# Performance work log

Hardware: AMD Instinct MI355X
Metric: run time of the kernel (lower is better)

The kernel has to match this reference:

```python
import jax, jax.numpy as jnp
import numpy as np

B, C, H, W = 8, 512, 32, 32
N_HEADS, HEAD_CH = 8, 64
INNER = N_HEADS * HEAD_CH  # 512
GROUPS = 32
EPS = 1e-5


def setup_inputs() -> dict:
    key = jax.random.key(0)
    ks = jax.random.split(key, 12)
    s = 0.02
    return {
        "x": jax.random.normal(ks[0], (B, C, H, W), jnp.float32),
        "c": jax.random.normal(ks[1], (B, C, H, W), jnp.float32),  # unused by module
        "gn_gamma": 1.0 + 0.1 * jax.random.normal(ks[2], (C,), jnp.float32),
        "gn_beta": 0.1 * jax.random.normal(ks[3], (C,), jnp.float32),
        "Wq": s * jax.random.normal(ks[4], (INNER, C), jnp.float32),
        "bq": s * jax.random.normal(ks[5], (INNER,), jnp.float32),
        "Wk": s * jax.random.normal(ks[6], (INNER, C), jnp.float32),
        "bk": s * jax.random.normal(ks[7], (INNER,), jnp.float32),
        "Wv": s * jax.random.normal(ks[8], (INNER, C), jnp.float32),
        "bv": s * jax.random.normal(ks[9], (INNER,), jnp.float32),
        "Wo": s * jax.random.normal(ks[10], (C, INNER), jnp.float32),
        "bo": s * jax.random.normal(ks[11], (C,), jnp.float32),
    }


def group_norm(x, gamma, beta):
    b, c, h, w = x.shape
    xg = x.reshape(b, GROUPS, c // GROUPS, h, w)
    mean = xg.mean(axis=(2, 3, 4), keepdims=True)
    var = xg.var(axis=(2, 3, 4), keepdims=True)
    xn = ((xg - mean) * jax.lax.rsqrt(var + EPS)).reshape(b, c, h, w)
    return xn * gamma[None, :, None, None] + beta[None, :, None, None]


def reference(x, c, gn_gamma, gn_beta, Wq, bq, Wk, bk, Wv, bv, Wo, bo):
    b, ch, h, w = x.shape
    L = h * w
    x_in = x
    xn = group_norm(x, gn_gamma, gn_beta).reshape(b, ch, L)  # b c l
    # 1x1 Conv1d == channel-wise linear
    q = jnp.einsum('oc,bcl->bol', Wq, xn) + bq[None, :, None]
    k = jnp.einsum('oc,bcl->bol', Wk, xn) + bk[None, :, None]
    v = jnp.einsum('oc,bcl->bol', Wv, xn) + bv[None, :, None]
    d = INNER // N_HEADS
    q = q.reshape(b * N_HEADS, d, L)
    k = k.reshape(b * N_HEADS, d, L)
    v = v.reshape(b * N_HEADS, d, L)
    scale = 1.0 / np.sqrt(np.sqrt(d))
    attn_map = jnp.einsum('bct,bcs->bts', q * scale, k * scale)  # (b*n) t s
    weight = jax.nn.softmax(attn_map.astype(jnp.float32), axis=-1).astype(attn_map.dtype)
    a = jnp.einsum('bts,bcs->bct', weight, v)  # (b*n) d t
    a = a.reshape(b, INNER, L)
    out = jnp.einsum('oc,bcl->bol', Wo, a) + bo[None, :, None]
    out = out.reshape(b, ch, h, w) + x_in
    return out, attn_map
```

## Files before the change

kernel.cpp:

```cpp
#include <hip/hip_runtime.h>
#include <math.h>

#define B_      8
#define C_      512
#define L_      1024
#define NH_     8
#define D_      64
#define BH_     64
#define GROUPS_ 32
#define CPG_    16
#define EPS_    1e-5f

typedef __attribute__((ext_vector_type(8))) short bf16x8;
typedef __attribute__((ext_vector_type(4))) float f32x4;

__device__ __forceinline__ unsigned short f2bf(float f) {
  union { float f; unsigned u; } v; v.f = f;
  unsigned r = v.u + 0x7FFFu + ((v.u >> 16) & 1u);
  return (unsigned short)(r >> 16);
}

__device__ __forceinline__ void gload_lds16(const unsigned short* g,
                                            unsigned short* l) {
  __builtin_amdgcn_global_load_lds(
      (const __attribute__((address_space(1))) void*)g,
      (__attribute__((address_space(3))) void*)l, 16, 0, 0);
}

__global__ void __launch_bounds__(256) gn_kernel(
    const float* __restrict__ x, const float* __restrict__ gamma,
    const float* __restrict__ beta, unsigned short* __restrict__ xn_t) {
  int b = blockIdx.x >> 5, g = blockIdx.x & 31;
  int tid = threadIdx.x;
  const float* xp = x + ((size_t)b * C_ + g * CPG_) * L_;
  f32x4 vals[CPG_];
  float s = 0.f, ss = 0.f;
#pragma unroll
  for (int c = 0; c < CPG_; ++c) {
    f32x4 v = *(const f32x4*)&xp[(size_t)c * L_ + tid * 4];
    vals[c] = v;
    s  += v[0] + v[1] + v[2] + v[3];
    ss += v[0] * v[0] + v[1] * v[1] + v[2] * v[2] + v[3] * v[3];
  }
  __shared__ float red0[256], red1[256];
  red0[tid] = s; red1[tid] = ss;
  __syncthreads();
  for (int off = 128; off > 0; off >>= 1) {
    if (tid < off) { red0[tid] += red0[tid + off]; red1[tid] += red1[tid + off]; }
    __syncthreads();
  }
  float mean = red0[0] * (1.f / 16384.f);
  float var  = red1[0] * (1.f / 16384.f) - mean * mean;
  float rstd = rsqrtf(var + EPS_);
  float gm[CPG_], bt[CPG_];
#pragma unroll
  for (int c = 0; c < CPG_; ++c) {
    gm[c] = gamma[g * CPG_ + c]; bt[c] = beta[g * CPG_ + c];
  }
#pragma unroll
  for (int r = 0; r < 4; ++r) {
    int l = tid * 4 + r;
    unsigned short obuf[16];
#pragma unroll
    for (int c = 0; c < CPG_; ++c)
      obuf[c] = f2bf((vals[c][r] - mean) * rstd * gm[c] + bt[c]);
    unsigned short* dst = xn_t + ((size_t)b * L_ + l) * C_ + g * CPG_;
    *(bf16x8*)dst       = *(bf16x8*)obuf;
    *(bf16x8*)(dst + 8) = *(bf16x8*)(obuf + 8);
  }
}

__global__ void __launch_bounds__(256) cast_w_kernel(
    const float* __restrict__ w0, const float* __restrict__ w1,
    const float* __restrict__ w2, const float* __restrict__ w3,
    unsigned short* __restrict__ o0, unsigned short* __restrict__ o1,
    unsigned short* __restrict__ o2, unsigned short* __restrict__ o3) {
  const float* src; unsigned short* dst; float sc;
  switch (blockIdx.y) {
    case 0: src = w0; dst = o0; sc = 0.125f; break;
    case 1: src = w1; dst = o1; sc = 1.f; break;
    case 2: src = w2; dst = o2; sc = 1.f; break;
    default: src = w3; dst = o3; sc = 1.f; break;
  }
  int i = (blockIdx.x * 256 + threadIdx.x) * 4;
  float4 v = *(const float4*)(src + i);
  unsigned short o[4] = {f2bf(v.x * sc), f2bf(v.y * sc), f2bf(v.z * sc), f2bf(v.w * sc)};
  *(unsigned long long*)(dst + i) = *(unsigned long long*)o;
}

template<int BM, bool BIAS_COL, bool BIAS_ROW, bool OUT_F32, bool RESID, bool DUAL>
__global__ void __launch_bounds__(256) mfma_gemm(
    const unsigned short* __restrict__ A,
    const unsigned short* __restrict__ B0, const unsigned short* __restrict__ B1,
    void* __restrict__ D0, void* __restrict__ D1,
    const float* __restrict__ bias0, const float* __restrict__ bias1,
    float bs0, float bs1, const float* __restrict__ resid,
    int K, int lda, int ldb, int ldd, int zdiv,
    long sAi, long sBi, long sDi) {
  constexpr int BN = 128, BK = 64;
  constexpr int MI = BM / 32;
  constexpr int WM = BM / 2;
  constexpr int RPW_A = BM / 4;
  __shared__ unsigned short As[BM * BK];
  __shared__ unsigned short Bs[BN * BK];
  int tid = threadIdx.x;
  int wave = tid >> 6, lane = tid & 63;
  int lm = lane & 15, q = lane >> 4;
  int wm = wave >> 1, wn = wave & 1;
  int m0 = blockIdx.x * BM, n0 = blockIdx.y * BN;
  int z = blockIdx.z, zo = z / zdiv, zi = z % zdiv;

  const unsigned short* Ab = A + (size_t)zi * sAi;
  const unsigned short* Bb = ((DUAL && zo) ? B1 : B0) + (size_t)zi * sBi;
  void* Dv = (DUAL && zo) ? D1 : D0;
  const float* bias = (DUAL && zo) ? bias1 : bias0;
  float bscale = (DUAL && zo) ? bs1 : bs0;

  f32x4 acc[MI][4];
#pragma unroll
  for (int mi = 0; mi < MI; ++mi)
#pragma unroll
    for (int ni = 0; ni < 4; ++ni) acc[mi][ni] = (f32x4){0.f, 0.f, 0.f, 0.f};

  int ly = lane >> 3;
  int lx = (lane & 7) * 8;

  for (int k0 = 0; k0 < K; k0 += BK) {
#pragma unroll
    for (int j = 0; j < BM / 32; ++j) {
      int r0 = wave * RPW_A + j * 8;
      gload_lds16(&Ab[(size_t)(m0 + r0 + ly) * lda + k0 + lx], &As[r0 * BK]);
    }
#pragma unroll
    for (int j = 0; j < 4; ++j) {
      int r0 = wave * 32 + j * 8;
      gload_lds16(&Bb[(size_t)(n0 + r0 + ly) * ldb + k0 + lx], &Bs[r0 * BK]);
    }
    __syncthreads();
#pragma unroll
    for (int kk = 0; kk < 2; ++kk) {
      bf16x8 af[MI], bfr[4];
#pragma unroll
      for (int mi = 0; mi < MI; ++mi)
        af[mi] = *(const bf16x8*)&As[(wm * WM + mi * 16 + lm) * BK + kk * 32 + q * 8];
#pragma unroll
      for (int ni = 0; ni < 4; ++ni)
        bfr[ni] = *(const bf16x8*)&Bs[(wn * 64 + ni * 16 + lm) * BK + kk * 32 + q * 8];
#pragma unroll
      for (int mi = 0; mi < MI; ++mi)
#pragma unroll
        for (int ni = 0; ni < 4; ++ni)
          acc[mi][ni] = __builtin_amdgcn_mfma_f32_16x16x32_bf16(
              af[mi], bfr[ni], acc[mi][ni], 0, 0, 0);
    }
    __syncthreads();
  }

  float* Df = (float*)Dv + (size_t)zi * sDi;
  unsigned short* Dh = (unsigned short*)Dv + (size_t)zi * sDi;
  const float* Rb = RESID ? resid + (size_t)zi * sDi : (const float*)0;
#pragma unroll
  for (int mi = 0; mi < MI; ++mi) {
#pragma unroll
    for (int ni = 0; ni < 4; ++ni) {
      int n = n0 + wn * 64 + ni * 16 + lm;
      float bc = BIAS_COL ? bias[n] * bscale : 0.f;
#pragma unroll
      for (int r = 0; r < 4; ++r) {
        int m = m0 + wm * WM + mi * 16 + q * 4 + r;
        float v = acc[mi][ni][r];
        if (BIAS_COL) v += bc;
        if (BIAS_ROW) v += bias[m] * bscale;
        size_t idx = (size_t)m * ldd + n;
        if (RESID) v += Rb[idx];
        if (OUT_F32) Df[idx] = v;
        else Dh[idx] = f2bf(v);
      }
    }
  }
}

#define PKF 72
#define PPF 80
__global__ void __launch_bounds__(256) flash_kernel(
    const unsigned short* __restrict__ q_t, const unsigned short* __restrict__ k_t,
    const unsigned short* __restrict__ v, float* __restrict__ attn,
    unsigned short* __restrict__ a_t) {
  __shared__ unsigned short Ks[64 * PKF];
  __shared__ unsigned short Vs[64 * PKF];
  __shared__ unsigned short Ps[4 * 32 * PPF];
  int tid = threadIdx.x, wave = tid >> 6, lane = tid & 63;
  int lm = lane & 15, q = lane >> 4;
  int bh = blockIdx.x, b = bh >> 3, h = bh & 7;
  int t0 = blockIdx.y * 128;
  int tw = t0 + wave * 32;
  const unsigned short* qb = q_t + (size_t)b * L_ * C_ + h * 64;
  const unsigned short* kb = k_t + (size_t)b * L_ * C_ + h * 64;
  const unsigned short* vb = v + ((size_t)b * C_ + h * 64) * L_;
  float* Sb = attn + (size_t)bh * L_ * L_;
  unsigned short* ab = a_t + (size_t)b * L_ * C_ + h * 64;
  unsigned short* Pw = Ps + wave * 32 * PPF;

  bf16x8 aq[2][2];
#pragma unroll
  for (int mi = 0; mi < 2; ++mi)
#pragma unroll
    for (int kk = 0; kk < 2; ++kk)
      aq[mi][kk] = *(const bf16x8*)&qb[(size_t)(tw + mi * 16 + lm) * C_ + kk * 32 + q * 8];

  f32x4 acc_o[2][4];
  float l_i[2][4];
#pragma unroll
  for (int mi = 0; mi < 2; ++mi)
#pragma unroll
    for (int r = 0; r < 4; ++r) l_i[mi][r] = 0.f;
#pragma unroll
  for (int mi = 0; mi < 2; ++mi)
#pragma unroll
    for (int ni = 0; ni < 4; ++ni) acc_o[mi][ni] = (f32x4){0.f, 0.f, 0.f, 0.f};

  int srow = tid >> 2, scol = (tid & 3) * 16;

  bf16x8 kp0 = *(const bf16x8*)&kb[(size_t)srow * C_ + scol];
  bf16x8 kp1 = *(const bf16x8*)&kb[(size_t)srow * C_ + scol + 8];
  bf16x8 vp0 = *(const bf16x8*)&vb[(size_t)srow * L_ + scol];
  bf16x8 vp1 = *(const bf16x8*)&vb[(size_t)srow * L_ + scol + 8];

  for (int s0 = 0; s0 < L_; s0 += 64) {
    __syncthreads();
    *(bf16x8*)&Ks[srow * PKF + scol]     = kp0;
    *(bf16x8*)&Ks[srow * PKF + scol + 8] = kp1;
    *(bf16x8*)&Vs[srow * PKF + scol]     = vp0;
    *(bf16x8*)&Vs[srow * PKF + scol + 8] = vp1;
    __syncthreads();

    if (s0 + 64 < L_) {
      int s1 = s0 + 64;
      kp0 = *(const bf16x8*)&kb[(size_t)(s1 + srow) * C_ + scol];
      kp1 = *(const bf16x8*)&kb[(size_t)(s1 + srow) * C_ + scol + 8];
      vp0 = *(const bf16x8*)&vb[(size_t)srow * L_ + s1 + scol];
      vp1 = *(const bf16x8*)&vb[(size_t)srow * L_ + s1 + scol + 8];
    }

    f32x4 acc_s[2][4];
#pragma unroll
    for (int mi = 0; mi < 2; ++mi)
#pragma unroll
      for (int ni = 0; ni < 4; ++ni) acc_s[mi][ni] = (f32x4){0.f, 0.f, 0.f, 0.f};
    __builtin_amdgcn_s_setprio(1);
#pragma unroll
    for (int kk = 0; kk < 2; ++kk) {
      bf16x8 bk[4];
#pragma unroll
      for (int ni = 0; ni < 4; ++ni)
        bk[ni] = *(const bf16x8*)&Ks[(ni * 16 + lm) * PKF + kk * 32 + q * 8];
#pragma unroll
      for (int mi = 0; mi < 2; ++mi)
#pragma unroll
        for (int ni = 0; ni < 4; ++ni)
          acc_s[mi][ni] = __builtin_amdgcn_mfma_f32_16x16x32_bf16(
              aq[mi][kk], bk[ni], acc_s[mi][ni], 0, 0, 0);
    }
    __builtin_amdgcn_s_setprio(0);

#pragma unroll
    for (int mi = 0; mi < 2; ++mi) {
#pragma unroll
      for (int r = 0; r < 4; ++r) {
        int t = tw + mi * 16 + q * 4 + r;
        float* So = &Sb[(size_t)t * L_ + s0];
        float ps = 0.f;
#pragma unroll
        for (int ni = 0; ni < 4; ++ni) {
          float sv = acc_s[mi][ni][r];
          So[ni * 16 + lm] = sv;
          float p = __expf(sv);
          ps += p;
          acc_s[mi][ni][r] = p;
        }
        l_i[mi][r] += ps;
#pragma unroll
        for (int ni = 0; ni < 4; ++ni)
          Pw[(mi * 16 + q * 4 + r) * PPF + ni * 16 + lm] = f2bf(acc_s[mi][ni][r]);
      }
    }

    __builtin_amdgcn_s_setprio(1);
#pragma unroll
    for (int kk = 0; kk < 2; ++kk) {
      bf16x8 ap[2], bv4[4];
#pragma unroll
      for (int mi = 0; mi < 2; ++mi)
        ap[mi] = *(const bf16x8*)&Pw[(mi * 16 + lm) * PPF + kk * 32 + q * 8];
#pragma unroll
      for (int ni = 0; ni < 4; ++ni)
        bv4[ni] = *(const bf16x8*)&Vs[(ni * 16 + lm) * PKF + kk * 32 + q * 8];
#pragma unroll
      for (int mi = 0; mi < 2; ++mi)
#pragma unroll
        for (int ni = 0; ni < 4; ++ni)
          acc_o[mi][ni] = __builtin_amdgcn_mfma_f32_16x16x32_bf16(
              ap[mi], bv4[ni], acc_o[mi][ni], 0, 0, 0);
    }
    __builtin_amdgcn_s_setprio(0);
  }

#pragma unroll
  for (int mi = 0; mi < 2; ++mi) {
#pragma unroll
    for (int r = 0; r < 4; ++r) {
      float lf = l_i[mi][r];
      lf += __shfl_xor(lf, 1);
      lf += __shfl_xor(lf, 2);
      lf += __shfl_xor(lf, 4);
      lf += __shfl_xor(lf, 8);
      float rinv = 1.0f / lf;
      int t = tw + mi * 16 + q * 4 + r;
#pragma unroll
      for (int ni = 0; ni < 4; ++ni)
        ab[(size_t)t * C_ + ni * 16 + lm] = f2bf(acc_o[mi][ni][r] * rinv);
    }
  }
}

extern "C" void kernel_launch(void* const* d_in, const int* in_sizes, int n_in,
                              void* d_out, int out_size, void* d_ws, size_t ws_size,
                              hipStream_t stream) {
  const float* x   = (const float*)d_in[0];
  const float* gam = (const float*)d_in[2];
  const float* bet = (const float*)d_in[3];
  const float* Wq  = (const float*)d_in[4];
  const float* bq  = (const float*)d_in[5];
  const float* Wk  = (const float*)d_in[6];
  const float* bk  = (const float*)d_in[7];
  const float* Wv  = (const float*)d_in[8];
  const float* bv  = (const float*)d_in[9];
  const float* Wo  = (const float*)d_in[10];
  const float* bo  = (const float*)d_in[11];

  const size_t NE = (size_t)B_ * C_ * L_;
  float* out  = (float*)d_out;
  float* attn = out + NE;

  char* ws = (char*)d_ws;
  unsigned short* xn_t = (unsigned short*)(ws);
  unsigned short* q_t  = (unsigned short*)(ws + 8388608);
  unsigned short* k_t  = (unsigned short*)(ws + 16777216);
  unsigned short* v    = (unsigned short*)(ws + 25165824);
  unsigned short* a_t  = (unsigned short*)(ws + 33554432);
  unsigned short* wqb  = (unsigned short*)(ws + 41943040);
  unsigned short* wkb  = (unsigned short*)(ws + 42467328);
  unsigned short* wvb  = (unsigned short*)(ws + 42991616);
  unsigned short* wob  = (unsigned short*)(ws + 43515904);

  const long SBL = (long)C_ * L_;

  gn_kernel<<<B_ * GROUPS_, 256, 0, stream>>>(x, gam, bet, xn_t);
  cast_w_kernel<<<dim3(256, 4), 256, 0, stream>>>(Wq, Wk, Wv, Wo, wqb, wkb, wvb, wob);

  mfma_gemm<128, true, false, false, false, true><<<dim3(64, 4, 2), 256, 0, stream>>>(
      xn_t, wqb, wkb, q_t, k_t, bq, bk, 0.125f, 1.f, nullptr,
      512, 512, 512, 512, 1, 0, 0, 0);
  mfma_gemm<64, false, true, false, false, false><<<dim3(8, 8, 8), 256, 0, stream>>>(
      wvb, xn_t, nullptr, v, nullptr, bv, nullptr, 1.f, 1.f, nullptr,
      512, 512, 512, 1024, 8, 0, SBL, SBL);

  flash_kernel<<<dim3(BH_, 8), 256, 0, stream>>>(q_t, k_t, v, attn, a_t);

  mfma_gemm<64, false, true, true, true, false><<<dim3(8, 8, 8), 256, 0, stream>>>(
      wob, a_t, nullptr, out, nullptr, bo, nullptr, 1.f, 1.f, x,
      512, 512, 512, 1024, 8, 0, SBL, SBL);
}
```

Measured before the change: 399.2 us.

## Transpose QK^T MFMA for vectorized nontemporal attn-map stores; fuse GN and weight cast

The score MFMA swaps its operands to compute K·Q^T, so each lane holds four contiguous key columns of one query row. That lets the 256MB fp32 attention map be written with 16-byte nontemporal stores instead of scattered scalar stores, and lets P be written to LDS as packed 8-byte chunks. The row-sum reduction is reworked to match the new layout. The GN and weight-cast kernels are merged into one launch, and the output GEMM's fp32 stores become nontemporal. The risk is extra shuffles in the epilogue and a changed LDS write pattern for P.

```diff
diff --git a/kernel.cpp b/kernel.cpp
--- a/kernel.cpp
+++ b/kernel.cpp
@@ -27,11 +27,36 @@
       (__attribute__((address_space(3))) void*)l, 16, 0, 0);
 }
 
-__global__ void __launch_bounds__(256) gn_kernel(
+__global__ void __launch_bounds__(256) gn_cast_kernel(
     const float* __restrict__ x, const float* __restrict__ gamma,
-    const float* __restrict__ beta, unsigned short* __restrict__ xn_t) {
-  int b = blockIdx.x >> 5, g = blockIdx.x & 31;
+    const float* __restrict__ beta, unsigned short* __restrict__ xn_t,
+    const float* __restrict__ w0, const float* __restrict__ w1,
+    const float* __restrict__ w2, const float* __restrict__ w3,
+    unsigned short* __restrict__ o0, unsigned short* __restrict__ o1,
+    unsigned short* __restrict__ o2, unsigned short* __restrict__ o3) {
+  int bid = blockIdx.x;
   int tid = threadIdx.x;
+  if (bid >= 256) {
+    int cb = bid - 256;
+    const float* src; unsigned short* dst; float sc;
+    switch (cb >> 6) {
+      case 0:  src = w0; dst = o0; sc = 0.125f; break;
+      case 1:  src = w1; dst = o1; sc = 1.f; break;
+      case 2:  src = w2; dst = o2; sc = 1.f; break;
+      default: src = w3; dst = o3; sc = 1.f; break;
+    }
+    int base = (cb & 63) * 4096 + tid * 4;
+#pragma unroll
+    for (int j = 0; j < 4; ++j) {
+      int i = base + j * 1024;
+      float4 v = *(const float4*)(src + i);
+      unsigned short o[4] = {f2bf(v.x * sc), f2bf(v.y * sc),
+                             f2bf(v.z * sc), f2bf(v.w * sc)};
+      *(unsigned long long*)(dst + i) = *(unsigned long long*)o;
+    }
+    return;
+  }
+  int b = bid >> 5, g = bid & 31;
   const float* xp = x + ((size_t)b * C_ + g * CPG_) * L_;
   f32x4 vals[CPG_];
   float s = 0.f, ss = 0.f;
@@ -68,24 +93,6 @@
     *(bf16x8*)dst       = *(bf16x8*)obuf;
     *(bf16x8*)(dst + 8) = *(bf16x8*)(obuf + 8);
   }
-}
-
-__global__ void __launch_bounds__(256) cast_w_kernel(
-    const float* __restrict__ w0, const float* __restrict__ w1,
-    const float* __restrict__ w2, const float* __restrict__ w3,
-    unsigned short* __restrict__ o0, unsigned short* __restrict__ o1,
-    unsigned short* __restrict__ o2, unsigned short* __restrict__ o3) {
-  const float* src; unsigned short* dst; float sc;
-  switch (blockIdx.y) {
-    case 0: src = w0; dst = o0; sc = 0.125f; break;
-    case 1: src = w1; dst = o1; sc = 1.f; break;
-    case 2: src = w2; dst = o2; sc = 1.f; break;
-    default: src = w3; dst = o3; sc = 1.f; break;
-  }
-  int i = (blockIdx.x * 256 + threadIdx.x) * 4;
-  float4 v = *(const float4*)(src + i);
-  unsigned short o[4] = {f2bf(v.x * sc), f2bf(v.y * sc), f2bf(v.z * sc), f2bf(v.w * sc)};
-  *(unsigned long long*)(dst + i) = *(unsigned long long*)o;
 }
 
 template<int BM, bool BIAS_COL, bool BIAS_ROW, bool OUT_F32, bool RESID, bool DUAL>
@@ -173,7 +180,7 @@
         if (BIAS_ROW) v += bias[m] * bscale;
         size_t idx = (size_t)m * ldd + n;
         if (RESID) v += Rb[idx];
-        if (OUT_F32) Df[idx] = v;
+        if (OUT_F32) __builtin_nontemporal_store(v, &Df[idx]);
         else Dh[idx] = f2bf(v);
       }
     }
@@ -203,17 +210,13 @@
 
   bf16x8 aq[2][2];
 #pragma unroll
-  for (int mi = 0; mi < 2; ++mi)
+  for (int tn = 0; tn < 2; ++tn)
 #pragma unroll
     for (int kk = 0; kk < 2; ++kk)
-      aq[mi][kk] = *(const bf16x8*)&qb[(size_t)(tw + mi * 16 + lm) * C_ + kk * 32 + q * 8];
+      aq[tn][kk] = *(const bf16x8*)&qb[(size_t)(tw + tn * 16 + lm) * C_ + kk * 32 + q * 8];
 
   f32x4 acc_o[2][4];
-  float l_i[2][4];
-#pragma unroll
-  for (int mi = 0; mi < 2; ++mi)
-#pragma unroll
-    for (int r = 0; r < 4; ++r) l_i[mi][r] = 0.f;
+  float l_i[2] = {0.f, 0.f};
 #pragma unroll
   for (int mi = 0; mi < 2; ++mi)
 #pragma unroll
@@ -242,47 +245,46 @@
       vp1 = *(const bf16x8*)&vb[(size_t)srow * L_ + s1 + scol + 8];
     }
 
-    f32x4 acc_s[2][4];
-#pragma unroll
-    for (int mi = 0; mi < 2; ++mi)
-#pragma unroll
-      for (int ni = 0; ni < 4; ++ni) acc_s[mi][ni] = (f32x4){0.f, 0.f, 0.f, 0.f};
+    f32x4 acc_st[4][2];
+#pragma unroll
+    for (int si = 0; si < 4; ++si)
+#pragma unroll
+      for (int tn = 0; tn < 2; ++tn) acc_st[si][tn] = (f32x4){0.f, 0.f, 0.f, 0.f};
     __builtin_amdgcn_s_setprio(1);
 #pragma unroll
     for (int kk = 0; kk < 2; ++kk) {
-      bf16x8 bk[4];
-#pragma unroll
-      for (int ni = 0; ni < 4; ++ni)
-        bk[ni] = *(const bf16x8*)&Ks[(ni * 16 + lm) * PKF + kk * 32 + q * 8];
-#pragma unroll
-      for (int mi = 0; mi < 2; ++mi)
-#pragma unroll
-        for (int ni = 0; ni < 4; ++ni)
-          acc_s[mi][ni] = __builtin_amdgcn_mfma_f32_16x16x32_bf16(
-              aq[mi][kk], bk[ni], acc_s[mi][ni], 0, 0, 0);
+      bf16x8 ak[4];
+#pragma unroll
+      for (int si = 0; si < 4; ++si)
+        ak[si] = *(const bf16x8*)&Ks[(si * 16 + lm) * PKF + kk * 32 + q * 8];
+#pragma unroll
+      for (int si = 0; si < 4; ++si)
+#pragma unroll
+        for (int tn = 0; tn < 2; ++tn)
+          acc_st[si][tn] = __builtin_amdgcn_mfma_f32_16x16x32_bf16(
+              ak[si], aq[tn][kk], acc_st[si][tn], 0, 0, 0);
     }
     __builtin_amdgcn_s_setprio(0);
 
 #pragma unroll
-    for (int mi = 0; mi < 2; ++mi) {
-#pragma unroll
-      for (int r = 0; r < 4; ++r) {
-        int t = tw + mi * 16 + q * 4 + r;
-        float* So = &Sb[(size_t)t * L_ + s0];
-        float ps = 0.f;
-#pragma unroll
-        for (int ni = 0; ni < 4; ++ni) {
-          float sv = acc_s[mi][ni][r];
-          So[ni * 16 + lm] = sv;
-          float p = __expf(sv);
-          ps += p;
-          acc_s[mi][ni][r] = p;
+    for (int tn = 0; tn < 2; ++tn) {
+      float* So = &Sb[(size_t)(tw + tn * 16 + lm) * L_ + s0 + q * 4];
+      float lsum = 0.f;
+#pragma unroll
+      for (int si = 0; si < 4; ++si) {
+        f32x4 sv = acc_st[si][tn];
+        __builtin_nontemporal_store(sv, (f32x4*)(So + si * 16));
+        unsigned short pk[4];
+#pragma unroll
+        for (int r = 0; r < 4; ++r) {
+          float p = __expf(sv[r]);
+          lsum += p;
+          pk[r] = f2bf(p);
         }
-        l_i[mi][r] += ps;
-#pragma unroll
-        for (int ni = 0; ni < 4; ++ni)
-          Pw[(mi * 16 + q * 4 + r) * PPF + ni * 16 + lm] = f2bf(acc_s[mi][ni][r]);
+        *(unsigned long long*)&Pw[(tn * 16 + lm) * PPF + si * 16 + q * 4] =
+            *(unsigned long long*)pk;
       }
+      l_i[tn] += lsum;
     }
 
     __builtin_amdgcn_s_setprio(1);
@@ -306,15 +308,17 @@
   }
 
 #pragma unroll
+  for (int tn = 0; tn < 2; ++tn) {
+    float lf = l_i[tn];
+    lf += __shfl_xor(lf, 16);
+    lf += __shfl_xor(lf, 32);
+    l_i[tn] = lf;
+  }
+#pragma unroll
   for (int mi = 0; mi < 2; ++mi) {
 #pragma unroll
     for (int r = 0; r < 4; ++r) {
-      float lf = l_i[mi][r];
-      lf += __shfl_xor(lf, 1);
-      lf += __shfl_xor(lf, 2);
-      lf += __shfl_xor(lf, 4);
-      lf += __shfl_xor(lf, 8);
-      float rinv = 1.0f / lf;
+      float rinv = 1.0f / __shfl(l_i[mi], q * 4 + r);
       int t = tw + mi * 16 + q * 4 + r;
 #pragma unroll
       for (int ni = 0; ni < 4; ++ni)
@@ -355,8 +359,8 @@
 
   const long SBL = (long)C_ * L_;
 
-  gn_kernel<<<B_ * GROUPS_, 256, 0, stream>>>(x, gam, bet, xn_t);
-  cast_w_kernel<<<dim3(256, 4), 256, 0, stream>>>(Wq, Wk, Wv, Wo, wqb, wkb, wvb, wob);
+  gn_cast_kernel<<<512, 256, 0, stream>>>(x, gam, bet, xn_t,
+                                          Wq, Wk, Wv, Wo, wqb, wkb, wvb, wob);
 
   mfma_gemm<128, true, false, false, false, true><<<dim3(64, 4, 2), 256, 0, stream>>>(
       xn_t, wqb, wkb, q_t, k_t, bq, bk, 0.125f, 1.f, nullptr,
```

Result: slower. 449.7 us (+12.7%).
